# Performance work log

Hardware: AMD Instinct MI355X
Metric: run time of the kernel (lower is better)

Reference implementation:

```python
import jax, jax.numpy as jnp
import numpy as np

BATCH = 262144
CLUSTER = 100

def _boost_generators():
    # Standard Lorentz boost generators K_x, K_y, K_z (symmetric, metric (+,-,-,-)).
    K = np.zeros((3, 4, 4), dtype=np.float32)
    for j in range(3):
        K[j, 0, j + 1] = 1.0
        K[j, j + 1, 0] = 1.0
    return jnp.asarray(K)

def setup_inputs() -> dict:
    key = jax.random.key(0)
    k1, k2, k3, k4 = jax.random.split(key, 4)
    T = jax.random.normal(k1, (BATCH, CLUSTER, 4), dtype=jnp.float32)
    # build() initializes boosts/bias uniform[0,1) scaled by 0.33 (|b| < 1 => gamma real)
    Bo = jax.random.uniform(k2, (CLUSTER, 3), dtype=jnp.float32) * 0.33
    Bi = jax.random.uniform(k3, (1, 3), dtype=jnp.float32) * 0.33
    W = jax.random.uniform(k4, (CLUSTER, 1), dtype=jnp.float32)
    K_mats = _boost_generators()
    return {"T": T, "Bo": Bo, "Bi": Bi, "W": W, "K_mats": K_mats}

def _lorentz(x, boosts, K_mats, weights=None):
    # x: (batch, C, 4), boosts: (C, 3) -> (batch, 4)
    mag = jnp.sqrt(jnp.sum(boosts * boosts, axis=1, keepdims=True))  # (C,1)
    n = boosts / mag                                                  # (C,3)
    g = 1.0 / jnp.sqrt(1.0 - mag * mag)                               # (C,1) gamma
    nK = jnp.einsum('cj,jad->cad', n, K_mats)                         # (C,4,4)
    nK2 = jnp.einsum('cab,cbd->cad', nK, nK)                          # (C,4,4)
    B = (jnp.eye(4, dtype=x.dtype)[None]
         - (g * mag)[..., None] * nK
         + (g - 1.0)[..., None] * nK2)                                # (C,4,4)
    if weights is not None:
        B = weights[:, :, None] * B                                   # per-element scalar weight
    # sum over cluster of B_c @ x[:, c]
    return jnp.einsum('cad,bcd->ba', B, x)

def reference(T, Bo, Bi, W, K_mats):
    summed = _lorentz(T, Bo, K_mats, weights=W)            # (batch, 4)
    out = _lorentz(summed[:, None, :], Bi, K_mats)         # (batch, 4)
    return out.reshape(T.shape[0], 1, 4)
```

## Files before the change

### kernel.cpp

```cpp
#include <hip/hip_runtime.h>
#include <math.h>

#define BATCH   262144
#define CLUSTER 100

__device__ inline void boost_mat(float bx, float by, float bz, float B[4][4]) {
    float m2  = bx * bx + by * by + bz * bz;
    float mag = sqrtf(m2);
    float nx = bx / mag, ny = by / mag, nz = bz / mag;
    float g  = 1.0f / sqrtf(1.0f - mag * mag);
    float gm = g * mag;
    float gm1 = g - 1.0f;
    float n[3] = {nx, ny, nz};
    B[0][0] = 1.0f + gm1 * (nx * nx + ny * ny + nz * nz);
    for (int j = 0; j < 3; ++j) {
        B[0][j + 1] = -gm * n[j];
        B[j + 1][0] = -gm * n[j];
    }
    for (int i = 0; i < 3; ++i)
        for (int j = 0; j < 3; ++j)
            B[i + 1][j + 1] = ((i == j) ? 1.0f : 0.0f) + gm1 * n[i] * n[j];
}

__global__ void build_M_kernel(const float* __restrict__ Bo,
                               const float* __restrict__ Bi,
                               const float* __restrict__ W,
                               float* __restrict__ M) {
    int c = threadIdx.x;
    if (c >= CLUSTER) return;

    float BiM[4][4];
    boost_mat(Bi[0], Bi[1], Bi[2], BiM);

    float BoM[4][4];
    boost_mat(Bo[c * 3 + 0], Bo[c * 3 + 1], Bo[c * 3 + 2], BoM);

    float w = W[c];
    for (int a = 0; a < 4; ++a)
        for (int d = 0; d < 4; ++d) {
            float s = 0.0f;
            for (int e = 0; e < 4; ++e)
                s += BiM[a][e] * (w * BoM[e][d]);
            M[c * 16 + a * 4 + d] = s;
        }
}

__global__ __launch_bounds__(256, 4) void lorentz_main_kernel(
        const float* __restrict__ T,
        const float* __restrict__ M,
        float* __restrict__ out) {
    __shared__ float sM[CLUSTER * 16];

    int tid = threadIdx.x;
    for (int i = tid; i < CLUSTER * 4; i += 256)
        ((float4*)sM)[i] = ((const float4*)M)[i];
    __syncthreads();

    int wave = tid >> 6;
    int lane = tid & 63;
    int q  = lane & 3;
    int rl = lane >> 2;
    long long row = (long long)blockIdx.x * 64 + wave * 16 + rl;

    const float4* Trow = (const float4*)(T + row * (CLUSTER * 4));

    float ax = 0.0f, ay = 0.0f, az = 0.0f, aw = 0.0f;

    #pragma unroll 5
    for (int t = 0; t < 25; ++t) {
        int c = 4 * t + q;
        float4 v = Trow[t * 4 + q];
        const float4* m = (const float4*)(sM + c * 16);
        float4 m0 = m[0], m1 = m[1], m2 = m[2], m3 = m[3];
        ax += m0.x * v.x + m0.y * v.y + m0.z * v.z + m0.w * v.w;
        ay += m1.x * v.x + m1.y * v.y + m1.z * v.z + m1.w * v.w;
        az += m2.x * v.x + m2.y * v.y + m2.z * v.z + m2.w * v.w;
        aw += m3.x * v.x + m3.y * v.y + m3.z * v.z + m3.w * v.w;
    }

    ax += __shfl_xor(ax, 1); ax += __shfl_xor(ax, 2);
    ay += __shfl_xor(ay, 1); ay += __shfl_xor(ay, 2);
    az += __shfl_xor(az, 1); az += __shfl_xor(az, 2);
    aw += __shfl_xor(aw, 1); aw += __shfl_xor(aw, 2);

    if (q == 0) {
        float4 o = {ax, ay, az, aw};
        ((float4*)out)[row] = o;
    }
}

extern "C" void kernel_launch(void* const* d_in, const int* in_sizes, int n_in,
                              void* d_out, int out_size, void* d_ws, size_t ws_size,
                              hipStream_t stream) {
    const float* T  = (const float*)d_in[0];
    const float* Bo = (const float*)d_in[1];
    const float* Bi = (const float*)d_in[2];
    const float* W  = (const float*)d_in[3];

    float* M = (float*)d_ws;
    float* out = (float*)d_out;

    build_M_kernel<<<1, 128, 0, stream>>>(Bo, Bi, W, M);

    int blocks = BATCH / 64;
    lorentz_main_kernel<<<blocks, 256, 0, stream>>>(T, M, out);
}
```

Before: 88.55 us.

## Process four rows per thread group to reuse shared-memory matrix loads

Each 4-lane group now handles four batch rows instead of one, so every matrix block read from shared memory is reused across four input vectors, and the grid shrinks by a factor of four. All four lanes write an output row after the shuffle reduction instead of only lane 0. This cuts LDS traffic per row and adds memory-level parallelism per thread, at the cost of more registers, fewer waves, and strided global loads that span four rows.

After: 92.90 us. 1.05x slower.

```diff
diff --git a/kernel.cpp b/kernel.cpp
--- a/kernel.cpp
+++ b/kernel.cpp
@@ -45,6 +45,8 @@
         }
 }
 
+#define DOT4(mm, vv) ((mm).x*(vv).x + (mm).y*(vv).y + (mm).z*(vv).z + (mm).w*(vv).w)
+
 __global__ __launch_bounds__(256, 4) void lorentz_main_kernel(
         const float* __restrict__ T,
         const float* __restrict__ M,
@@ -59,34 +61,42 @@
     int wave = tid >> 6;
     int lane = tid & 63;
     int q  = lane & 3;
-    int rl = lane >> 2;
-    long long row = (long long)blockIdx.x * 64 + wave * 16 + rl;
+    int g  = lane >> 2;
+    long long rowBase = (long long)blockIdx.x * 256 + wave * 64 + g * 4;
 
-    const float4* Trow = (const float4*)(T + row * (CLUSTER * 4));
+    const float* T0 = T + rowBase * (CLUSTER * 4);
 
-    float ax = 0.0f, ay = 0.0f, az = 0.0f, aw = 0.0f;
+    float4 a0 = {0.f, 0.f, 0.f, 0.f};
+    float4 a1 = a0, a2 = a0, a3 = a0;
 
-    #pragma unroll 5
+    #pragma unroll 2
     for (int t = 0; t < 25; ++t) {
         int c = 4 * t + q;
-        float4 v = Trow[t * 4 + q];
+        float4 v0 = *(const float4*)(T0 +    0 + c * 4);
+        float4 v1 = *(const float4*)(T0 +  400 + c * 4);
+        float4 v2 = *(const float4*)(T0 +  800 + c * 4);
+        float4 v3 = *(const float4*)(T0 + 1200 + c * 4);
         const float4* m = (const float4*)(sM + c * 16);
         float4 m0 = m[0], m1 = m[1], m2 = m[2], m3 = m[3];
-        ax += m0.x * v.x + m0.y * v.y + m0.z * v.z + m0.w * v.w;
-        ay += m1.x * v.x + m1.y * v.y + m1.z * v.z + m1.w * v.w;
-        az += m2.x * v.x + m2.y * v.y + m2.z * v.z + m2.w * v.w;
-        aw += m3.x * v.x + m3.y * v.y + m3.z * v.z + m3.w * v.w;
+
+        a0.x += DOT4(m0, v0); a0.y += DOT4(m1, v0); a0.z += DOT4(m2, v0); a0.w += DOT4(m3, v0);
+        a1.x += DOT4(m0, v1); a1.y += DOT4(m1, v1); a1.z += DOT4(m2, v1); a1.w += DOT4(m3, v1);
+        a2.x += DOT4(m0, v2); a2.y += DOT4(m1, v2); a2.z += DOT4(m2, v2); a2.w += DOT4(m3, v2);
+        a3.x += DOT4(m0, v3); a3.y += DOT4(m1, v3); a3.z += DOT4(m2, v3); a3.w += DOT4(m3, v3);
     }
 
-    ax += __shfl_xor(ax, 1); ax += __shfl_xor(ax, 2);
-    ay += __shfl_xor(ay, 1); ay += __shfl_xor(ay, 2);
-    az += __shfl_xor(az, 1); az += __shfl_xor(az, 2);
-    aw += __shfl_xor(aw, 1); aw += __shfl_xor(aw, 2);
+    #define RED(f) f += __shfl_xor(f, 1); f += __shfl_xor(f, 2);
+    RED(a0.x) RED(a0.y) RED(a0.z) RED(a0.w)
+    RED(a1.x) RED(a1.y) RED(a1.z) RED(a1.w)
+    RED(a2.x) RED(a2.y) RED(a2.z) RED(a2.w)
+    RED(a3.x) RED(a3.y) RED(a3.z) RED(a3.w)
+    #undef RED
 
-    if (q == 0) {
-        float4 o = {ax, ay, az, aw};
-        ((float4*)out)[row] = o;
-    }
+    float4 o = a0;
+    if (q == 1) o = a1;
+    if (q == 2) o = a2;
+    if (q == 3) o = a3;
+    ((float4*)out)[rowBase + q] = o;
 }
 
 extern "C" void kernel_launch(void* const* d_in, const int* in_sizes, int n_in,
@@ -102,6 +112,6 @@
 
     build_M_kernel<<<1, 128, 0, stream>>>(Bo, Bi, W, M);
 
-    int blocks = BATCH / 64;
+    int blocks = BATCH / 256;
     lorentz_main_kernel<<<blocks, 256, 0, stream>>>(T, M, out);
 }
```
